# Performance work log

Measured on AMD Instinct MI355X. Metric: run time of the kernel, lower is better.

Reference implementation:

```python
import jax, jax.numpy as jnp
import numpy as np

B, T, D, H = 4, 1024, 1024, 16
NUM_BUCKETS = 320
MAX_DIST = 800
LN_EPS = 1e-5


def _rel_bucket(T):
    # bidirectional T5-style relative position buckets
    ctx = jnp.arange(T)[:, None]
    mem = jnp.arange(T)[None, :]
    rel = mem - ctx  # (T, T)
    half = NUM_BUCKETS // 2  # 160
    bucket = (rel > 0).astype(jnp.int32) * half
    n = jnp.abs(rel)
    max_exact = half // 2  # 80
    is_small = n < max_exact
    n_f = jnp.maximum(n, 1).astype(jnp.float32)
    large = max_exact + (
        jnp.log(n_f / max_exact) / np.log(MAX_DIST / max_exact) * (half - max_exact)
    ).astype(jnp.int32)
    large = jnp.minimum(large, half - 1)
    return bucket + jnp.where(is_small, n, large)


def setup_inputs() -> dict:
    key = jax.random.key(0)
    ks = jax.random.split(key, 12)
    s = 0.02
    return {
        "x": jax.random.normal(ks[0], (B, T, D), jnp.float32),
        "ln_w": jnp.ones((D,), jnp.float32),
        "ln_b": jnp.zeros((D,), jnp.float32),
        "wq": jax.random.normal(ks[1], (D, D), jnp.float32) * s,
        "bq": jnp.zeros((D,), jnp.float32),
        "wk": jax.random.normal(ks[2], (D, D), jnp.float32) * s,
        "bk": jnp.zeros((D,), jnp.float32),
        "wv": jax.random.normal(ks[3], (D, D), jnp.float32) * s,
        "bv": jnp.zeros((D,), jnp.float32),
        "wo": jax.random.normal(ks[4], (D, D), jnp.float32) * s,
        "bo": jnp.zeros((D,), jnp.float32),
        "rel_emb": jax.random.normal(ks[5], (NUM_BUCKETS, H), jnp.float32) * s,
        "grep_w": jax.random.normal(ks[6], (8, D // H), jnp.float32) * s,
        "grep_b": jnp.zeros((8,), jnp.float32),
        "grep_a": jnp.ones((1, H, 1, 1), jnp.float32),
    }


def reference(x, ln_w, ln_b, wq, bq, wk, bk, wv, bv, wo, bo, rel_emb, grep_w, grep_b, grep_a):
    Bb, Tt, Dd = x.shape
    hd = Dd // H
    scaling = hd ** -0.5
    # pre-norm LayerNorm
    mu = jnp.mean(x, -1, keepdims=True)
    var = jnp.mean((x - mu) ** 2, -1, keepdims=True)
    h = (x - mu) / jnp.sqrt(var + LN_EPS) * ln_w + ln_b
    # projections (q pre-scaled as in fairseq/WavLM)
    q = (h @ wq.T + bq) * scaling
    k = h @ wk.T + bk
    v = h @ wv.T + bv
    q = q.reshape(Bb, Tt, H, hd).transpose(0, 2, 1, 3)  # (B,H,T,hd)
    k = k.reshape(Bb, Tt, H, hd).transpose(0, 2, 1, 3)
    v = v.reshape(Bb, Tt, H, hd).transpose(0, 2, 1, 3)
    # bucketed relative position bias: (H, T, T)
    buckets = _rel_bucket(Tt)
    pos_bias = rel_emb[buckets].transpose(2, 0, 1)
    # gru_rel_pos gating (per batch, head, query position)
    alpha = 32.0
    ql = q * (alpha / scaling)  # undo scaling, multiply by alpha
    g = jax.nn.sigmoid((ql @ grep_w.T + grep_b).reshape(Bb, H, Tt, 2, 4).sum(-1))
    gate_a, gate_b = g[..., 0:1], g[..., 1:2]  # (B,H,T,1)
    gate = gate_a * (gate_b * grep_a - 1.0) + 2.0
    # attention
    scores = jnp.einsum('bhtd,bhsd->bhts', q, k) + gate * pos_bias[None]
    attn = jax.nn.softmax(scores, axis=-1)
    out = jnp.einsum('bhts,bhsd->bhtd', attn, v).transpose(0, 2, 1, 3).reshape(Bb, Tt, Dd)
    # output projection, dropout (identity in eval), residual
    out = out @ wo.T + bo + x
    pos_bias_out = jnp.broadcast_to(pos_bias[None], (Bb, H, Tt, Tt)).reshape(Bb * H, Tt, Tt)
    return out, pos_bias_out
```

## Files before the change

### kernel.cpp

```cpp
#include <hip/hip_runtime.h>

typedef unsigned short u16;
typedef __attribute__((ext_vector_type(8))) short short8;
typedef __attribute__((ext_vector_type(4))) float floatx4;

#define MFMA16(a, b, c) __builtin_amdgcn_mfma_f32_16x16x32_bf16(a, b, c, 0, 0, 0)

#define GLL16(gp, lp)                                                              \
  __builtin_amdgcn_global_load_lds(                                                \
      (const __attribute__((address_space(1))) void*)(gp),                         \
      (__attribute__((address_space(3))) void*)(lp), 16, 0, 0)

__device__ __forceinline__ float bf2f(u16 u) {
  return __uint_as_float(((unsigned int)u) << 16);
}
__device__ __forceinline__ u16 f2bf(float f) {
  unsigned int u = __float_as_uint(f);
  unsigned int r = (u + 0x7fffu + ((u >> 16) & 1u)) >> 16;
  return (u16)r;
}

__global__ __launch_bounds__(256) void ln_kernel(
    const float* __restrict__ x, const float* __restrict__ w, const float* __restrict__ bb,
    u16* __restrict__ hb)
{
  int wid = threadIdx.x >> 6, lane = threadIdx.x & 63;
  int row = blockIdx.x * 4 + wid;
  const float* xr = x + row * 1024 + lane * 16;
  float xs[16];
#pragma unroll
  for (int i = 0; i < 4; i++) {
    float4 v = *(const float4*)(xr + i * 4);
    xs[i * 4 + 0] = v.x; xs[i * 4 + 1] = v.y; xs[i * 4 + 2] = v.z; xs[i * 4 + 3] = v.w;
  }
  float s = 0.f, ss = 0.f;
#pragma unroll
  for (int i = 0; i < 16; i++) { s += xs[i]; ss += xs[i] * xs[i]; }
#pragma unroll
  for (int m = 1; m < 64; m <<= 1) { s += __shfl_xor(s, m, 64); ss += __shfl_xor(ss, m, 64); }
  float mu = s * (1.0f / 1024.0f);
  float var = ss * (1.0f / 1024.0f) - mu * mu;
  float rstd = rsqrtf(var + 1e-5f);
  const float* wr = w + lane * 16;
  const float* br = bb + lane * 16;
  short8 o0, o1;
#pragma unroll
  for (int i = 0; i < 8; i++) {
    o0[i] = (short)f2bf((xs[i] - mu) * rstd * wr[i] + br[i]);
    o1[i] = (short)f2bf((xs[8 + i] - mu) * rstd * wr[8 + i] + br[8 + i]);
  }
  u16* hr = hb + row * 1024 + lane * 16;
  *(short8*)hr = o0;
  *(short8*)(hr + 8) = o1;
}

__device__ __forceinline__ int rel_bucket(int t, int s) {
  int rel = s - t;
  int bucket = (rel > 0) ? 160 : 0;
  int n = (rel < 0) ? -rel : rel;
  if (n < 80) return bucket + n;
  float a = logf((float)n / 80.0f);
  float c = a / (float)2.302585092994046;
  float v = c * 80.0f;
  int large = 80 + (int)v;
  if (large > 159) large = 159;
  return bucket + large;
}

__global__ __launch_bounds__(256) void convw_kernel(
    const float* __restrict__ wq, const float* __restrict__ wk,
    const float* __restrict__ wv, const float* __restrict__ wo,
    u16* __restrict__ wb, const float* __restrict__ rel_emb, float* __restrict__ tbl)
{
  int bid = blockIdx.x;
  if (bid >= 2048) {
    int idx = (bid - 2048) * 256 + threadIdx.x;
    int h = idx & 15, ri = idx >> 4;
    float v = 0.f;
    if (ri < 2047) {
      int rel = ri - 1023;
      v = rel_emb[rel_bucket(0, rel) * 16 + h];
    }
    tbl[h * 2048 + ri] = v;
    return;
  }
  int idx = (bid * 256 + threadIdx.x) * 8;
  int seg = idx >> 20, off = idx & 1048575;
  const float* s = (seg == 0) ? wq : (seg == 1) ? wk : (seg == 2) ? wv : wo;
  float4 f0 = *(const float4*)(s + off);
  float4 f1 = *(const float4*)(s + off + 4);
  short8 o;
  o[0] = (short)f2bf(f0.x); o[1] = (short)f2bf(f0.y);
  o[2] = (short)f2bf(f0.z); o[3] = (short)f2bf(f0.w);
  o[4] = (short)f2bf(f1.x); o[5] = (short)f2bf(f1.y);
  o[6] = (short)f2bf(f1.z); o[7] = (short)f2bf(f1.w);
  *(short8*)&wb[idx] = o;
}

__global__ __launch_bounds__(256) void qkv_kernel(
    const u16* __restrict__ hb, const u16* __restrict__ wb,
    const float* __restrict__ bq, const float* __restrict__ bk, const float* __restrict__ bv,
    u16* __restrict__ qs, u16* __restrict__ kko, u16* __restrict__ vn)
{
  __shared__ __align__(16) u16 As[128 * 32];
  __shared__ __align__(16) u16 Bs[128 * 32];
  int tid = threadIdx.x;
  int wid = tid >> 6, lane = tid & 63;
  int wm = wid >> 1, wn = wid & 1;
  int l15 = lane & 15, quad = lane >> 4;
  int m0 = blockIdx.y * 128;
  int n0g = blockIdx.x * 128;
  int sec = n0g >> 10;
  int n0 = n0g & 1023;
  const u16* W = wb + sec * 1048576;
  const float* bias = (sec == 0) ? bq : ((sec == 1) ? bk : bv);

  floatx4 zero4 = {0.f, 0.f, 0.f, 0.f};
  floatx4 acc[4][4];
#pragma unroll
  for (int i = 0; i < 4; i++)
#pragma unroll
    for (int j = 0; j < 4; j++) acc[i][j] = zero4;

  int lr = tid >> 2;
  int lc = (tid & 3) * 8;
  const u16* ga0 = &hb[(m0 + lr) * 1024 + lc];
  const u16* ga1 = &hb[(m0 + lr + 64) * 1024 + lc];
  const u16* gb0 = &W[(n0 + lr) * 1024 + lc];
  const u16* gb1 = &W[(n0 + lr + 64) * 1024 + lc];
  u16* la0 = &As[lr * 32 + lc];
  u16* la1 = &As[(lr + 64) * 32 + lc];
  u16* lb0 = &Bs[lr * 32 + lc];
  u16* lb1 = &Bs[(lr + 64) * 32 + lc];

  for (int kt = 0; kt < 1024; kt += 32) {
    GLL16(ga0 + kt, la0);
    GLL16(ga1 + kt, la1);
    GLL16(gb0 + kt, lb0);
    GLL16(gb1 + kt, lb1);
    __syncthreads();
    short8 af[4], bf[4];
#pragma unroll
    for (int mi = 0; mi < 4; mi++)
      af[mi] = *(const short8*)&As[(wm * 64 + mi * 16 + l15) * 32 + quad * 8];
#pragma unroll
    for (int ni = 0; ni < 4; ni++)
      bf[ni] = *(const short8*)&Bs[(wn * 64 + ni * 16 + l15) * 32 + quad * 8];
#pragma unroll
    for (int mi = 0; mi < 4; mi++)
#pragma unroll
      for (int ni = 0; ni < 4; ni++)
        acc[mi][ni] = MFMA16(af[mi], bf[ni], acc[mi][ni]);
    __syncthreads();
  }

  int bidx = m0 >> 10;
#pragma unroll
  for (int mi = 0; mi < 4; mi++) {
#pragma unroll
    for (int ni = 0; ni < 4; ni++) {
#pragma unroll
      for (int r = 0; r < 4; r++) {
        int row = m0 + wm * 64 + mi * 16 + quad * 4 + r;
        int t = row & 1023;
        int c = n0 + wn * 64 + ni * 16 + l15;
        float val = acc[mi][ni][r] + bias[c];
        int hh = c >> 6, hp = c & 63;
        if (sec == 0) {
          val *= 0.125f;
          qs[((bidx * 16 + hh) * 1024 + t) * 64 + hp] = f2bf(val);
        } else if (sec == 1) {
          kko[((bidx * 16 + hh) * 1024 + t) * 64 + hp] = f2bf(val);
        } else {
          vn[((bidx * 16 + hh) * 1024 + t) * 64 + hp] = f2bf(val);
        }
      }
    }
  }
}

__global__ __launch_bounds__(256) void vtrans_kernel(
    const u16* __restrict__ vn, u16* __restrict__ vt)
{
  __shared__ u16 Ts[64 * 72];
  int bh = blockIdx.x >> 4;
  int t0 = (blockIdx.x & 15) * 64;
  int tid = threadIdx.x;
  int row = tid >> 2;
  int c16 = (tid & 3) * 16;
  const u16* src = vn + bh * 65536 + (t0 + row) * 64 + c16;
  *(short8*)&Ts[row * 72 + c16]     = *(const short8*)&src[0];
  *(short8*)&Ts[row * 72 + c16 + 8] = *(const short8*)&src[8];
  __syncthreads();
  short8 o0, o1;
#pragma unroll
  for (int j = 0; j < 8; j++) {
    o0[j] = (short)Ts[(c16 + j) * 72 + row];
    o1[j] = (short)Ts[(c16 + 8 + j) * 72 + row];
  }
  u16* dst = vt + bh * 65536 + row * 1024 + t0 + c16;
  *(short8*)&dst[0] = o0;
  *(short8*)&dst[8] = o1;
}

__global__ __launch_bounds__(256) void attn_kernel(
    const u16* __restrict__ qs, const u16* __restrict__ kko, const u16* __restrict__ vt,
    const float* __restrict__ gw, const float* __restrict__ gb, const float* __restrict__ ga,
    const float* __restrict__ tbl, u16* __restrict__ ao)
{
  __shared__ __align__(16) u16 Pb[4][2 * 768];
  int wid = threadIdx.x >> 6, lane = threadIdx.x & 63;
  int l15 = lane & 15, quad = lane >> 4;
  int bh = blockIdx.x;
  int b = bh >> 4, h = bh & 15;
  int q0 = blockIdx.y * 64 + wid * 16;
  const u16* Q = qs + bh * 65536;
  const u16* K = kko + bh * 65536;
  const u16* V = vt + bh * 65536;
  u16* pbase = &Pb[wid][0];

  const u16* qrow = Q + (q0 + l15) * 64;
  float e[8];
#pragma unroll
  for (int i = 0; i < 8; i++) e[i] = 0.f;
  {
    short8 qa = *(const short8*)&qrow[quad * 16];
    short8 qc = *(const short8*)&qrow[quad * 16 + 8];
#pragma unroll
    for (int jj = 0; jj < 8; jj++) {
      float qla = bf2f((u16)qa[jj]) * 256.0f;
      float qlb = bf2f((u16)qc[jj]) * 256.0f;
      int j = quad * 16 + jj;
#pragma unroll
      for (int i = 0; i < 8; i++) {
        e[i] += qla * gw[i * 64 + j];
        e[i] += qlb * gw[i * 64 + j + 8];
      }
    }
  }
#pragma unroll
  for (int i = 0; i < 8; i++) {
    e[i] += __shfl_xor(e[i], 16, 64);
    e[i] += __shfl_xor(e[i], 32, 64);
  }
  float u0 = e[0] + e[1] + e[2] + e[3] + gb[0] + gb[1] + gb[2] + gb[3];
  float u1 = e[4] + e[5] + e[6] + e[7] + gb[4] + gb[5] + gb[6] + gb[7];
  float sa = 1.0f / (1.0f + __expf(-u0));
  float sc_ = 1.0f / (1.0f + __expf(-u1));
  float gv = sa * (sc_ * ga[h] - 1.0f) + 2.0f;

  short8 qf0 = *(const short8*)&Q[(q0 + l15) * 64 + quad * 8];
  short8 qf1 = *(const short8*)&Q[(q0 + l15) * 64 + quad * 8 + 32];

  const float* tb = tbl + h * 2048 + 1023 + quad * 4 - (q0 + l15);

  float mrun = -1e30f, lrun = 0.f;
  floatx4 zero4 = {0.f, 0.f, 0.f, 0.f};
  floatx4 accO[4];
#pragma unroll
  for (int ni = 0; ni < 4; ni++) accO[ni] = zero4;

  const u16* Kr = K + l15 * 64 + quad * 8;
  short8 ka0 = *(const short8*)&Kr[0];
  short8 ka1 = *(const short8*)&Kr[32];
  short8 kb0 = *(const short8*)&Kr[16 * 64];
  short8 kb1 = *(const short8*)&Kr[16 * 64 + 32];
  float bt[8];
#pragma unroll
  for (int r = 0; r < 4; r++) { bt[r] = tb[r]; bt[4 + r] = tb[16 + r]; }

  for (int it = 0; it < 32; it++) {
    int s0 = it * 32;
    floatx4 sc0 = zero4, sc1 = zero4;
    sc0 = MFMA16(ka0, qf0, sc0);
    sc0 = MFMA16(ka1, qf1, sc0);
    sc1 = MFMA16(kb0, qf0, sc1);
    sc1 = MFMA16(kb1, qf1, sc1);

    int sn = (s0 + 32) & 1023;
    const u16* Kn = K + (sn + l15) * 64 + quad * 8;
    short8 na0 = *(const short8*)&Kn[0];
    short8 na1 = *(const short8*)&Kn[32];
    short8 nb0 = *(const short8*)&Kn[16 * 64];
    short8 nb1 = *(const short8*)&Kn[16 * 64 + 32];
    float btn[8];
#pragma unroll
    for (int r = 0; r < 4; r++) { btn[r] = tb[sn + r]; btn[4 + r] = tb[sn + 16 + r]; }
    short8 vf0 = *(const short8*)&V[(0 * 16 + l15) * 1024 + s0 + quad * 8];
    short8 vf1 = *(const short8*)&V[(1 * 16 + l15) * 1024 + s0 + quad * 8];
    short8 vf2 = *(const short8*)&V[(2 * 16 + l15) * 1024 + s0 + quad * 8];
    short8 vf3 = *(const short8*)&V[(3 * 16 + l15) * 1024 + s0 + quad * 8];

    float vv[8];
#pragma unroll
    for (int r = 0; r < 4; r++) {
      vv[r]     = sc0[r] + gv * bt[r];
      vv[4 + r] = sc1[r] + gv * bt[4 + r];
    }
    float mt = fmaxf(fmaxf(fmaxf(vv[0], vv[1]), fmaxf(vv[2], vv[3])),
                     fmaxf(fmaxf(vv[4], vv[5]), fmaxf(vv[6], vv[7])));
    mt = fmaxf(mt, __shfl_xor(mt, 16, 64));
    mt = fmaxf(mt, __shfl_xor(mt, 32, 64));
    float mnew = fmaxf(mrun, mt);
    float al = __expf(fmaxf(mrun - mnew, -80.0f));
    float p[8], ps = 0.f;
#pragma unroll
    for (int j = 0; j < 8; j++) { p[j] = __expf(vv[j] - mnew); ps += p[j]; }
    ps += __shfl_xor(ps, 16, 64);
    ps += __shfl_xor(ps, 32, 64);
    lrun = lrun * al + ps;
    mrun = mnew;

    float ar[4];
#pragma unroll
    for (int r = 0; r < 4; r++) ar[r] = __shfl(al, quad * 4 + r, 64);
#pragma unroll
    for (int ni = 0; ni < 4; ni++) {
      floatx4 t = accO[ni];
      t[0] *= ar[0]; t[1] *= ar[1]; t[2] *= ar[2]; t[3] *= ar[3];
      accO[ni] = t;
    }

    unsigned w0, w1, w2, w3;
    asm("v_cvt_pk_bf16_f32 %0, %1, %2" : "=v"(w0) : "v"(p[0]), "v"(p[1]));
    asm("v_cvt_pk_bf16_f32 %0, %1, %2" : "=v"(w1) : "v"(p[2]), "v"(p[3]));
    asm("v_cvt_pk_bf16_f32 %0, %1, %2" : "=v"(w2) : "v"(p[4]), "v"(p[5]));
    asm("v_cvt_pk_bf16_f32 %0, %1, %2" : "=v"(w3) : "v"(p[6]), "v"(p[7]));
    u16* pw = pbase + (it & 1) * 768;
    uint2 wa; wa.x = w0; wa.y = w1;
    uint2 wbv; wbv.x = w2; wbv.y = w3;
    *(uint2*)&pw[l15 * 48 + quad * 4] = wa;
    *(uint2*)&pw[l15 * 48 + 16 + quad * 4] = wbv;
    asm volatile("s_waitcnt lgkmcnt(0)" ::: "memory");
    __builtin_amdgcn_sched_barrier(0);
    short8 pf = *(const short8*)&pw[l15 * 48 + quad * 8];

    accO[0] = MFMA16(pf, vf0, accO[0]);
    accO[1] = MFMA16(pf, vf1, accO[1]);
    accO[2] = MFMA16(pf, vf2, accO[2]);
    accO[3] = MFMA16(pf, vf3, accO[3]);

    ka0 = na0; ka1 = na1; kb0 = nb0; kb1 = nb1;
#pragma unroll
    for (int j = 0; j < 8; j++) bt[j] = btn[j];
  }

#pragma unroll
  for (int r = 0; r < 4; r++) {
    float lr = __shfl(lrun, quad * 4 + r, 64);
    float rl = 1.0f / lr;
    int t = q0 + quad * 4 + r;
#pragma unroll
    for (int ni = 0; ni < 4; ni++) {
      ao[(b * 1024 + t) * 1024 + h * 64 + ni * 16 + l15] = f2bf(accO[ni][r] * rl);
    }
  }
}

__global__ __launch_bounds__(256) void oproj_kernel(
    const u16* __restrict__ ao, const u16* __restrict__ wob, const float* __restrict__ bo,
    const float* __restrict__ x, float* __restrict__ out)
{
  __shared__ __align__(16) u16 As[128 * 32];
  __shared__ __align__(16) u16 Bs[128 * 32];
  int tid = threadIdx.x;
  int wid = tid >> 6, lane = tid & 63;
  int wm = wid >> 1, wn = wid & 1;
  int l15 = lane & 15, quad = lane >> 4;
  int m0 = blockIdx.y * 128;
  int n0 = blockIdx.x * 128;

  floatx4 zero4 = {0.f, 0.f, 0.f, 0.f};
  floatx4 acc[4][4];
#pragma unroll
  for (int i = 0; i < 4; i++)
#pragma unroll
    for (int j = 0; j < 4; j++) acc[i][j] = zero4;

  int lr = tid >> 2;
  int lc = (tid & 3) * 8;
  const u16* ga0 = &ao[(m0 + lr) * 1024 + lc];
  const u16* ga1 = &ao[(m0 + lr + 64) * 1024 + lc];
  const u16* gb0 = &wob[(n0 + lr) * 1024 + lc];
  const u16* gb1 = &wob[(n0 + lr + 64) * 1024 + lc];
  u16* la0 = &As[lr * 32 + lc];
  u16* la1 = &As[(lr + 64) * 32 + lc];
  u16* lb0 = &Bs[lr * 32 + lc];
  u16* lb1 = &Bs[(lr + 64) * 32 + lc];

  for (int kt = 0; kt < 1024; kt += 32) {
    GLL16(ga0 + kt, la0);
    GLL16(ga1 + kt, la1);
    GLL16(gb0 + kt, lb0);
    GLL16(gb1 + kt, lb1);
    __syncthreads();
    short8 af[4], bf[4];
#pragma unroll
    for (int mi = 0; mi < 4; mi++)
      af[mi] = *(const short8*)&As[(wm * 64 + mi * 16 + l15) * 32 + quad * 8];
#pragma unroll
    for (int ni = 0; ni < 4; ni++)
      bf[ni] = *(const short8*)&Bs[(wn * 64 + ni * 16 + l15) * 32 + quad * 8];
#pragma unroll
    for (int mi = 0; mi < 4; mi++)
#pragma unroll
      for (int ni = 0; ni < 4; ni++)
        acc[mi][ni] = MFMA16(af[mi], bf[ni], acc[mi][ni]);
    __syncthreads();
  }

#pragma unroll
  for (int mi = 0; mi < 4; mi++) {
#pragma unroll
    for (int ni = 0; ni < 4; ni++) {
#pragma unroll
      for (int r = 0; r < 4; r++) {
        int row = m0 + wm * 64 + mi * 16 + quad * 4 + r;
        int c = n0 + wn * 64 + ni * 16 + l15;
        out[row * 1024 + c] = acc[mi][ni][r] + bo[c] + x[row * 1024 + c];
      }
    }
  }
}

__global__ __launch_bounds__(256) void bias_all_kernel(
    const float* __restrict__ rel_emb, float* __restrict__ out1)
{
  int tid = blockIdx.x * 256 + threadIdx.x;
  int t = tid >> 7;
  int s0 = (tid & 127) * 8;
  int bkt[8];
#pragma unroll
  for (int j = 0; j < 8; j++) bkt[j] = rel_bucket(t, s0 + j) * 16;
  int base_ts = t * 1024 + s0;
#pragma unroll
  for (int hh = 0; hh < 16; hh++) {
    float4 v0, v1;
    v0.x = rel_emb[bkt[0] + hh]; v0.y = rel_emb[bkt[1] + hh];
    v0.z = rel_emb[bkt[2] + hh]; v0.w = rel_emb[bkt[3] + hh];
    v1.x = rel_emb[bkt[4] + hh]; v1.y = rel_emb[bkt[5] + hh];
    v1.z = rel_emb[bkt[6] + hh]; v1.w = rel_emb[bkt[7] + hh];
    float* p = out1 + hh * 1048576 + base_ts;
    *(float4*)p = v0;              *(float4*)(p + 4) = v1;
    *(float4*)(p + 16777216) = v0; *(float4*)(p + 16777216 + 4) = v1;
    *(float4*)(p + 33554432) = v0; *(float4*)(p + 33554432 + 4) = v1;
    *(float4*)(p + 50331648) = v0; *(float4*)(p + 50331648 + 4) = v1;
  }
}

extern "C" void kernel_launch(void* const* d_in, const int* in_sizes, int n_in,
                              void* d_out, int out_size, void* d_ws, size_t ws_size,
                              hipStream_t stream) {
  const float* x    = (const float*)d_in[0];
  const float* ln_w = (const float*)d_in[1];
  const float* ln_b = (const float*)d_in[2];
  const float* wq   = (const float*)d_in[3];
  const float* bq   = (const float*)d_in[4];
  const float* wk   = (const float*)d_in[5];
  const float* bk   = (const float*)d_in[6];
  const float* wv   = (const float*)d_in[7];
  const float* bv   = (const float*)d_in[8];
  const float* wo   = (const float*)d_in[9];
  const float* bo   = (const float*)d_in[10];
  const float* rel  = (const float*)d_in[11];
  const float* gw   = (const float*)d_in[12];
  const float* gb   = (const float*)d_in[13];
  const float* ga   = (const float*)d_in[14];

  float* out0  = (float*)d_out;
  float* out1f = out0 + 4194304;

  u16* hbb  = (u16*)(out1f + 16777216);
  u16* wbb  = (u16*)(out1f + 18874368);
  u16* qsb  = (u16*)(out1f + 20971520);
  u16* kkb  = (u16*)(out1f + 23068672);
  u16* vnb  = (u16*)(out1f + 25165824);
  u16* vtb  = (u16*)(out1f + 27262976);
  u16* aob  = (u16*)(out1f + 29360128);
  float* tbl =        out1f + 31457280;

  ln_kernel<<<1024, 256, 0, stream>>>(x, ln_w, ln_b, hbb);
  convw_kernel<<<2176, 256, 0, stream>>>(wq, wk, wv, wo, wbb, rel, tbl);
  qkv_kernel<<<dim3(24, 32), 256, 0, stream>>>(hbb, wbb, bq, bk, bv, qsb, kkb, vnb);
  vtrans_kernel<<<1024, 256, 0, stream>>>(vnb, vtb);
  attn_kernel<<<dim3(64, 16), 256, 0, stream>>>(qsb, kkb, vtb, gw, gb, ga, tbl, aob);
  oproj_kernel<<<dim3(8, 32), 256, 0, stream>>>(aob, wbb + 3145728, bo, x, out0);
  bias_all_kernel<<<512, 256, 0, stream>>>(rel, out1f);
}
```

Baseline: 524.6 us.

## Fold positional-bias output writes into QKV and attention kernels as extra blocks

When the workspace is large enough, intermediates move from the tail of the output buffer into the workspace. The standalone bias broadcast kernel, which writes 256 MB, is then split across extra blocks appended to the QKV GEMM grid (256 blocks) and the attention grid (256 blocks). The aim is to overlap the bandwidth-bound bias stores with compute-bound GEMM and attention work and to remove one launch. The risk is that the store traffic competes with the compute blocks for memory bandwidth and cache. If the workspace is too small, the old path runs unchanged.

```diff
diff --git a/kernel.cpp b/kernel.cpp
--- a/kernel.cpp
+++ b/kernel.cpp
@@ -18,40 +18,6 @@
   unsigned int u = __float_as_uint(f);
   unsigned int r = (u + 0x7fffu + ((u >> 16) & 1u)) >> 16;
   return (u16)r;
-}
-
-__global__ __launch_bounds__(256) void ln_kernel(
-    const float* __restrict__ x, const float* __restrict__ w, const float* __restrict__ bb,
-    u16* __restrict__ hb)
-{
-  int wid = threadIdx.x >> 6, lane = threadIdx.x & 63;
-  int row = blockIdx.x * 4 + wid;
-  const float* xr = x + row * 1024 + lane * 16;
-  float xs[16];
-#pragma unroll
-  for (int i = 0; i < 4; i++) {
-    float4 v = *(const float4*)(xr + i * 4);
-    xs[i * 4 + 0] = v.x; xs[i * 4 + 1] = v.y; xs[i * 4 + 2] = v.z; xs[i * 4 + 3] = v.w;
-  }
-  float s = 0.f, ss = 0.f;
-#pragma unroll
-  for (int i = 0; i < 16; i++) { s += xs[i]; ss += xs[i] * xs[i]; }
-#pragma unroll
-  for (int m = 1; m < 64; m <<= 1) { s += __shfl_xor(s, m, 64); ss += __shfl_xor(ss, m, 64); }
-  float mu = s * (1.0f / 1024.0f);
-  float var = ss * (1.0f / 1024.0f) - mu * mu;
-  float rstd = rsqrtf(var + 1e-5f);
-  const float* wr = w + lane * 16;
-  const float* br = bb + lane * 16;
-  short8 o0, o1;
-#pragma unroll
-  for (int i = 0; i < 8; i++) {
-    o0[i] = (short)f2bf((xs[i] - mu) * rstd * wr[i] + br[i]);
-    o1[i] = (short)f2bf((xs[8 + i] - mu) * rstd * wr[8 + i] + br[8 + i]);
-  }
-  u16* hr = hb + row * 1024 + lane * 16;
-  *(short8*)hr = o0;
-  *(short8*)(hr + 8) = o1;
 }
 
 __device__ __forceinline__ int rel_bucket(int t, int s) {
@@ -67,6 +33,65 @@
   return bucket + large;
 }
 
+__device__ __forceinline__ void bias_slice(int bid, const float* __restrict__ rel_emb,
+                                           float* __restrict__ out1)
+{
+  int tid = bid * 256 + threadIdx.x;
+  int t = tid >> 7;
+  int s0 = (tid & 127) * 8;
+  int bkt[8];
+#pragma unroll
+  for (int j = 0; j < 8; j++) bkt[j] = rel_bucket(t, s0 + j) * 16;
+  int base_ts = t * 1024 + s0;
+#pragma unroll
+  for (int hh = 0; hh < 16; hh++) {
+    float4 v0, v1;
+    v0.x = rel_emb[bkt[0] + hh]; v0.y = rel_emb[bkt[1] + hh];
+    v0.z = rel_emb[bkt[2] + hh]; v0.w = rel_emb[bkt[3] + hh];
+    v1.x = rel_emb[bkt[4] + hh]; v1.y = rel_emb[bkt[5] + hh];
+    v1.z = rel_emb[bkt[6] + hh]; v1.w = rel_emb[bkt[7] + hh];
+    float* p = out1 + hh * 1048576 + base_ts;
+    *(float4*)p = v0;              *(float4*)(p + 4) = v1;
+    *(float4*)(p + 16777216) = v0; *(float4*)(p + 16777216 + 4) = v1;
+    *(float4*)(p + 33554432) = v0; *(float4*)(p + 33554432 + 4) = v1;
+    *(float4*)(p + 50331648) = v0; *(float4*)(p + 50331648 + 4) = v1;
+  }
+}
+
+__global__ __launch_bounds__(256) void ln_kernel(
+    const float* __restrict__ x, const float* __restrict__ w, const float* __restrict__ bb,
+    u16* __restrict__ hb)
+{
+  int wid = threadIdx.x >> 6, lane = threadIdx.x & 63;
+  int row = blockIdx.x * 4 + wid;
+  const float* xr = x + row * 1024 + lane * 16;
+  float xs[16];
+#pragma unroll
+  for (int i = 0; i < 4; i++) {
+    float4 v = *(const float4*)(xr + i * 4);
+    xs[i * 4 + 0] = v.x; xs[i * 4 + 1] = v.y; xs[i * 4 + 2] = v.z; xs[i * 4 + 3] = v.w;
+  }
+  float s = 0.f, ss = 0.f;
+#pragma unroll
+  for (int i = 0; i < 16; i++) { s += xs[i]; ss += xs[i] * xs[i]; }
+#pragma unroll
+  for (int m = 1; m < 64; m <<= 1) { s += __shfl_xor(s, m, 64); ss += __shfl_xor(ss, m, 64); }
+  float mu = s * (1.0f / 1024.0f);
+  float var = ss * (1.0f / 1024.0f) - mu * mu;
+  float rstd = rsqrtf(var + 1e-5f);
+  const float* wr = w + lane * 16;
+  const float* br = bb + lane * 16;
+  short8 o0, o1;
+#pragma unroll
+  for (int i = 0; i < 8; i++) {
+    o0[i] = (short)f2bf((xs[i] - mu) * rstd * wr[i] + br[i]);
+    o1[i] = (short)f2bf((xs[8 + i] - mu) * rstd * wr[8 + i] + br[8 + i]);
+  }
+  u16* hr = hb + row * 1024 + lane * 16;
+  *(short8*)hr = o0;
+  *(short8*)(hr + 8) = o1;
+}
+
 __global__ __launch_bounds__(256) void convw_kernel(
     const float* __restrict__ wq, const float* __restrict__ wk,
     const float* __restrict__ wv, const float* __restrict__ wo,
@@ -100,10 +125,15 @@
 __global__ __launch_bounds__(256) void qkv_kernel(
     const u16* __restrict__ hb, const u16* __restrict__ wb,
     const float* __restrict__ bq, const float* __restrict__ bk, const float* __restrict__ bv,
-    u16* __restrict__ qs, u16* __restrict__ kko, u16* __restrict__ vn)
+    u16* __restrict__ qs, u16* __restrict__ kko, u16* __restrict__ vn,
+    const float* __restrict__ rel_emb, float* __restrict__ out1)
 {
   __shared__ __align__(16) u16 As[128 * 32];
   __shared__ __align__(16) u16 Bs[128 * 32];
+  if (blockIdx.x >= 24) {
+    bias_slice((blockIdx.x - 24) * gridDim.y + blockIdx.y, rel_emb, out1);
+    return;
+  }
   int tid = threadIdx.x;
   int wid = tid >> 6, lane = tid & 63;
   int wm = wid >> 1, wn = wid & 1;
@@ -206,9 +236,14 @@
 __global__ __launch_bounds__(256) void attn_kernel(
     const u16* __restrict__ qs, const u16* __restrict__ kko, const u16* __restrict__ vt,
     const float* __restrict__ gw, const float* __restrict__ gb, const float* __restrict__ ga,
-    const float* __restrict__ tbl, u16* __restrict__ ao)
+    const float* __restrict__ tbl, u16* __restrict__ ao,
+    const float* __restrict__ rel_emb, float* __restrict__ out1)
 {
   __shared__ __align__(16) u16 Pb[4][2 * 768];
+  if (blockIdx.x >= 64) {
+    bias_slice(256 + (blockIdx.x - 64) * gridDim.y + blockIdx.y, rel_emb, out1);
+    return;
+  }
   int wid = threadIdx.x >> 6, lane = threadIdx.x & 63;
   int l15 = lane & 15, quad = lane >> 4;
   int bh = blockIdx.x;
@@ -426,26 +461,7 @@
 __global__ __launch_bounds__(256) void bias_all_kernel(
     const float* __restrict__ rel_emb, float* __restrict__ out1)
 {
-  int tid = blockIdx.x * 256 + threadIdx.x;
-  int t = tid >> 7;
-  int s0 = (tid & 127) * 8;
-  int bkt[8];
-#pragma unroll
-  for (int j = 0; j < 8; j++) bkt[j] = rel_bucket(t, s0 + j) * 16;
-  int base_ts = t * 1024 + s0;
-#pragma unroll
-  for (int hh = 0; hh < 16; hh++) {
-    float4 v0, v1;
-    v0.x = rel_emb[bkt[0] + hh]; v0.y = rel_emb[bkt[1] + hh];
-    v0.z = rel_emb[bkt[2] + hh]; v0.w = rel_emb[bkt[3] + hh];
-    v1.x = rel_emb[bkt[4] + hh]; v1.y = rel_emb[bkt[5] + hh];
-    v1.z = rel_emb[bkt[6] + hh]; v1.w = rel_emb[bkt[7] + hh];
-    float* p = out1 + hh * 1048576 + base_ts;
-    *(float4*)p = v0;              *(float4*)(p + 4) = v1;
-    *(float4*)(p + 16777216) = v0; *(float4*)(p + 16777216 + 4) = v1;
-    *(float4*)(p + 33554432) = v0; *(float4*)(p + 33554432 + 4) = v1;
-    *(float4*)(p + 50331648) = v0; *(float4*)(p + 50331648 + 4) = v1;
-  }
+  bias_slice(blockIdx.x, rel_emb, out1);
 }
 
 extern "C" void kernel_launch(void* const* d_in, const int* in_sizes, int n_in,
@@ -470,20 +486,30 @@
   float* out0  = (float*)d_out;
   float* out1f = out0 + 4194304;
 
-  u16* hbb  = (u16*)(out1f + 16777216);
-  u16* wbb  = (u16*)(out1f + 18874368);
-  u16* qsb  = (u16*)(out1f + 20971520);
-  u16* kkb  = (u16*)(out1f + 23068672);
-  u16* vnb  = (u16*)(out1f + 25165824);
-  u16* vtb  = (u16*)(out1f + 27262976);
-  u16* aob  = (u16*)(out1f + 29360128);
-  float* tbl =        out1f + 31457280;
+  bool use_ws = (ws_size >= (size_t)(64u << 20));
+  float* scr = use_ws ? (float*)d_ws : (out1f + 16777216);
+
+  u16* hbb  = (u16*)(scr);
+  u16* wbb  = (u16*)(scr + 2097152);
+  u16* qsb  = (u16*)(scr + 4194304);
+  u16* kkb  = (u16*)(scr + 6291456);
+  u16* vnb  = (u16*)(scr + 8388608);
+  u16* vtb  = (u16*)(scr + 10485760);
+  u16* aob  = (u16*)(scr + 12582912);
+  float* tbl =        scr + 14680064;
 
   ln_kernel<<<1024, 256, 0, stream>>>(x, ln_w, ln_b, hbb);
   convw_kernel<<<2176, 256, 0, stream>>>(wq, wk, wv, wo, wbb, rel, tbl);
-  qkv_kernel<<<dim3(24, 32), 256, 0, stream>>>(hbb, wbb, bq, bk, bv, qsb, kkb, vnb);
-  vtrans_kernel<<<1024, 256, 0, stream>>>(vnb, vtb);
-  attn_kernel<<<dim3(64, 16), 256, 0, stream>>>(qsb, kkb, vtb, gw, gb, ga, tbl, aob);
-  oproj_kernel<<<dim3(8, 32), 256, 0, stream>>>(aob, wbb + 3145728, bo, x, out0);
-  bias_all_kernel<<<512, 256, 0, stream>>>(rel, out1f);
-}
+  if (use_ws) {
+    qkv_kernel<<<dim3(32, 32), 256, 0, stream>>>(hbb, wbb, bq, bk, bv, qsb, kkb, vnb, rel, out1f);
+    vtrans_kernel<<<1024, 256, 0, stream>>>(vnb, vtb);
+    attn_kernel<<<dim3(80, 16), 256, 0, stream>>>(qsb, kkb, vtb, gw, gb, ga, tbl, aob, rel, out1f);
+    oproj_kernel<<<dim3(8, 32), 256, 0, stream>>>(aob, wbb + 3145728, bo, x, out0);
+  } else {
+    qkv_kernel<<<dim3(24, 32), 256, 0, stream>>>(hbb, wbb, bq, bk, bv, qsb, kkb, vnb, rel, out1f);
+    vtrans_kernel<<<1024, 256, 0, stream>>>(vnb, vtb);
+    attn_kernel<<<dim3(64, 16), 256, 0, stream>>>(qsb, kkb, vtb, gw, gb, ga, tbl, aob, rel, out1f);
+    oproj_kernel<<<dim3(8, 32), 256, 0, stream>>>(aob, wbb + 3145728, bo, x, out0);
+    bias_all_kernel<<<512, 256, 0, stream>>>(rel, out1f);
+  }
+}
```

Result: slower. 560.3 us (+6.8%).

## Process 64 keys per attention iteration with lazy softmax rescaling

Applied to the files above, without the earlier changes.

The attention loop now handles 64 keys per iteration instead of 32, with two K fragment sets prefetched in a rotating fashion and twice as many V fragments loaded per step. The online softmax skips the max update and accumulator rescale when every lane's new tile max stays within 8 of the running max. The kernel gains a launch-bounds occupancy hint of 4, and scratch buffers move to the workspace when it is large enough. The intent is to cut per-key loop overhead, shuffles and rescale multiplies, at the cost of more registers and a larger LDS P buffer.

```diff
diff --git a/kernel.cpp b/kernel.cpp
--- a/kernel.cpp
+++ b/kernel.cpp
@@ -18,40 +18,6 @@
   unsigned int u = __float_as_uint(f);
   unsigned int r = (u + 0x7fffu + ((u >> 16) & 1u)) >> 16;
   return (u16)r;
-}
-
-__global__ __launch_bounds__(256) void ln_kernel(
-    const float* __restrict__ x, const float* __restrict__ w, const float* __restrict__ bb,
-    u16* __restrict__ hb)
-{
-  int wid = threadIdx.x >> 6, lane = threadIdx.x & 63;
-  int row = blockIdx.x * 4 + wid;
-  const float* xr = x + row * 1024 + lane * 16;
-  float xs[16];
-#pragma unroll
-  for (int i = 0; i < 4; i++) {
-    float4 v = *(const float4*)(xr + i * 4);
-    xs[i * 4 + 0] = v.x; xs[i * 4 + 1] = v.y; xs[i * 4 + 2] = v.z; xs[i * 4 + 3] = v.w;
-  }
-  float s = 0.f, ss = 0.f;
-#pragma unroll
-  for (int i = 0; i < 16; i++) { s += xs[i]; ss += xs[i] * xs[i]; }
-#pragma unroll
-  for (int m = 1; m < 64; m <<= 1) { s += __shfl_xor(s, m, 64); ss += __shfl_xor(ss, m, 64); }
-  float mu = s * (1.0f / 1024.0f);
-  float var = ss * (1.0f / 1024.0f) - mu * mu;
-  float rstd = rsqrtf(var + 1e-5f);
-  const float* wr = w + lane * 16;
-  const float* br = bb + lane * 16;
-  short8 o0, o1;
-#pragma unroll
-  for (int i = 0; i < 8; i++) {
-    o0[i] = (short)f2bf((xs[i] - mu) * rstd * wr[i] + br[i]);
-    o1[i] = (short)f2bf((xs[8 + i] - mu) * rstd * wr[8 + i] + br[8 + i]);
-  }
-  u16* hr = hb + row * 1024 + lane * 16;
-  *(short8*)hr = o0;
-  *(short8*)(hr + 8) = o1;
 }
 
 __device__ __forceinline__ int rel_bucket(int t, int s) {
@@ -65,6 +31,40 @@
   int large = 80 + (int)v;
   if (large > 159) large = 159;
   return bucket + large;
+}
+
+__global__ __launch_bounds__(256) void ln_kernel(
+    const float* __restrict__ x, const float* __restrict__ w, const float* __restrict__ bb,
+    u16* __restrict__ hb)
+{
+  int wid = threadIdx.x >> 6, lane = threadIdx.x & 63;
+  int row = blockIdx.x * 4 + wid;
+  const float* xr = x + row * 1024 + lane * 16;
+  float xs[16];
+#pragma unroll
+  for (int i = 0; i < 4; i++) {
+    float4 v = *(const float4*)(xr + i * 4);
+    xs[i * 4 + 0] = v.x; xs[i * 4 + 1] = v.y; xs[i * 4 + 2] = v.z; xs[i * 4 + 3] = v.w;
+  }
+  float s = 0.f, ss = 0.f;
+#pragma unroll
+  for (int i = 0; i < 16; i++) { s += xs[i]; ss += xs[i] * xs[i]; }
+#pragma unroll
+  for (int m = 1; m < 64; m <<= 1) { s += __shfl_xor(s, m, 64); ss += __shfl_xor(ss, m, 64); }
+  float mu = s * (1.0f / 1024.0f);
+  float var = ss * (1.0f / 1024.0f) - mu * mu;
+  float rstd = rsqrtf(var + 1e-5f);
+  const float* wr = w + lane * 16;
+  const float* br = bb + lane * 16;
+  short8 o0, o1;
+#pragma unroll
+  for (int i = 0; i < 8; i++) {
+    o0[i] = (short)f2bf((xs[i] - mu) * rstd * wr[i] + br[i]);
+    o1[i] = (short)f2bf((xs[8 + i] - mu) * rstd * wr[8 + i] + br[8 + i]);
+  }
+  u16* hr = hb + row * 1024 + lane * 16;
+  *(short8*)hr = o0;
+  *(short8*)(hr + 8) = o1;
 }
 
 __global__ __launch_bounds__(256) void convw_kernel(
@@ -203,12 +203,12 @@
   *(short8*)&dst[8] = o1;
 }
 
-__global__ __launch_bounds__(256) void attn_kernel(
+__global__ __launch_bounds__(256, 4) void attn_kernel(
     const u16* __restrict__ qs, const u16* __restrict__ kko, const u16* __restrict__ vt,
     const float* __restrict__ gw, const float* __restrict__ gb, const float* __restrict__ ga,
     const float* __restrict__ tbl, u16* __restrict__ ao)
 {
-  __shared__ __align__(16) u16 Pb[4][2 * 768];
+  __shared__ __align__(16) u16 Pb[4][2 * 1152];
   int wid = threadIdx.x >> 6, lane = threadIdx.x & 63;
   int l15 = lane & 15, quad = lane >> 4;
   int bh = blockIdx.x;
@@ -260,89 +260,108 @@
 #pragma unroll
   for (int ni = 0; ni < 4; ni++) accO[ni] = zero4;
 
-  const u16* Kr = K + l15 * 64 + quad * 8;
-  short8 ka0 = *(const short8*)&Kr[0];
-  short8 ka1 = *(const short8*)&Kr[32];
-  short8 kb0 = *(const short8*)&Kr[16 * 64];
-  short8 kb1 = *(const short8*)&Kr[16 * 64 + 32];
-  float bt[8];
-#pragma unroll
-  for (int r = 0; r < 4; r++) { bt[r] = tb[r]; bt[4 + r] = tb[16 + r]; }
-
-  for (int it = 0; it < 32; it++) {
-    int s0 = it * 32;
-    floatx4 sc0 = zero4, sc1 = zero4;
-    sc0 = MFMA16(ka0, qf0, sc0);
-    sc0 = MFMA16(ka1, qf1, sc0);
-    sc1 = MFMA16(kb0, qf0, sc1);
-    sc1 = MFMA16(kb1, qf1, sc1);
-
-    int sn = (s0 + 32) & 1023;
-    const u16* Kn = K + (sn + l15) * 64 + quad * 8;
-    short8 na0 = *(const short8*)&Kn[0];
-    short8 na1 = *(const short8*)&Kn[32];
-    short8 nb0 = *(const short8*)&Kn[16 * 64];
-    short8 nb1 = *(const short8*)&Kn[16 * 64 + 32];
-    float btn[8];
-#pragma unroll
-    for (int r = 0; r < 4; r++) { btn[r] = tb[sn + r]; btn[4 + r] = tb[sn + 16 + r]; }
-    short8 vf0 = *(const short8*)&V[(0 * 16 + l15) * 1024 + s0 + quad * 8];
-    short8 vf1 = *(const short8*)&V[(1 * 16 + l15) * 1024 + s0 + quad * 8];
-    short8 vf2 = *(const short8*)&V[(2 * 16 + l15) * 1024 + s0 + quad * 8];
-    short8 vf3 = *(const short8*)&V[(3 * 16 + l15) * 1024 + s0 + quad * 8];
-
-    float vv[8];
+  const u16* Kq8 = K + quad * 8;
+  short8 kc0 = *(const short8*)&Kq8[(0 + l15) * 64];
+  short8 kc1 = *(const short8*)&Kq8[(0 + l15) * 64 + 32];
+  short8 kc2 = *(const short8*)&Kq8[(16 + l15) * 64];
+  short8 kc3 = *(const short8*)&Kq8[(16 + l15) * 64 + 32];
+  short8 kn0 = *(const short8*)&Kq8[(32 + l15) * 64];
+  short8 kn1 = *(const short8*)&Kq8[(32 + l15) * 64 + 32];
+  short8 kn2 = *(const short8*)&Kq8[(48 + l15) * 64];
+  short8 kn3 = *(const short8*)&Kq8[(48 + l15) * 64 + 32];
+
+  for (int it = 0; it < 16; it++) {
+    int s0 = it * 64;
+    floatx4 sA0 = zero4, sA1 = zero4, sB0 = zero4, sB1 = zero4;
+    sA0 = MFMA16(kc0, qf0, sA0); sA0 = MFMA16(kc1, qf1, sA0);
+    sA1 = MFMA16(kc2, qf0, sA1); sA1 = MFMA16(kc3, qf1, sA1);
+    {
+      int sn = (s0 + 64) & 1023;
+      const u16* KA = K + (sn + l15) * 64 + quad * 8;
+      kc0 = *(const short8*)&KA[0];
+      kc1 = *(const short8*)&KA[32];
+      kc2 = *(const short8*)&KA[16 * 64];
+      kc3 = *(const short8*)&KA[16 * 64 + 32];
+    }
+    sB0 = MFMA16(kn0, qf0, sB0); sB0 = MFMA16(kn1, qf1, sB0);
+    sB1 = MFMA16(kn2, qf0, sB1); sB1 = MFMA16(kn3, qf1, sB1);
+    {
+      int sn = (s0 + 96) & 1023;
+      const u16* KB = K + (sn + l15) * 64 + quad * 8;
+      kn0 = *(const short8*)&KB[0];
+      kn1 = *(const short8*)&KB[32];
+      kn2 = *(const short8*)&KB[16 * 64];
+      kn3 = *(const short8*)&KB[16 * 64 + 32];
+    }
+    short8 vfA[4], vfB[4];
+#pragma unroll
+    for (int ni = 0; ni < 4; ni++) {
+      vfA[ni] = *(const short8*)&V[(ni * 16 + l15) * 1024 + s0 + quad * 8];
+      vfB[ni] = *(const short8*)&V[(ni * 16 + l15) * 1024 + s0 + 32 + quad * 8];
+    }
+
+    float vv[16];
 #pragma unroll
     for (int r = 0; r < 4; r++) {
-      vv[r]     = sc0[r] + gv * bt[r];
-      vv[4 + r] = sc1[r] + gv * bt[4 + r];
-    }
-    float mt = fmaxf(fmaxf(fmaxf(vv[0], vv[1]), fmaxf(vv[2], vv[3])),
-                     fmaxf(fmaxf(vv[4], vv[5]), fmaxf(vv[6], vv[7])));
+      vv[r]      = sA0[r] + gv * tb[s0 + r];
+      vv[4 + r]  = sA1[r] + gv * tb[s0 + 16 + r];
+      vv[8 + r]  = sB0[r] + gv * tb[s0 + 32 + r];
+      vv[12 + r] = sB1[r] + gv * tb[s0 + 48 + r];
+    }
+    float m0v = fmaxf(fmaxf(fmaxf(vv[0], vv[1]), fmaxf(vv[2], vv[3])),
+                      fmaxf(fmaxf(vv[4], vv[5]), fmaxf(vv[6], vv[7])));
+    float m1v = fmaxf(fmaxf(fmaxf(vv[8], vv[9]), fmaxf(vv[10], vv[11])),
+                      fmaxf(fmaxf(vv[12], vv[13]), fmaxf(vv[14], vv[15])));
+    float mt = fmaxf(m0v, m1v);
     mt = fmaxf(mt, __shfl_xor(mt, 16, 64));
     mt = fmaxf(mt, __shfl_xor(mt, 32, 64));
-    float mnew = fmaxf(mrun, mt);
-    float al = __expf(fmaxf(mrun - mnew, -80.0f));
-    float p[8], ps = 0.f;
-#pragma unroll
-    for (int j = 0; j < 8; j++) { p[j] = __expf(vv[j] - mnew); ps += p[j]; }
-    ps += __shfl_xor(ps, 16, 64);
-    ps += __shfl_xor(ps, 32, 64);
-    lrun = lrun * al + ps;
-    mrun = mnew;
-
-    float ar[4];
-#pragma unroll
-    for (int r = 0; r < 4; r++) ar[r] = __shfl(al, quad * 4 + r, 64);
-#pragma unroll
-    for (int ni = 0; ni < 4; ni++) {
-      floatx4 t = accO[ni];
-      t[0] *= ar[0]; t[1] *= ar[1]; t[2] *= ar[2]; t[3] *= ar[3];
-      accO[ni] = t;
-    }
-
-    unsigned w0, w1, w2, w3;
-    asm("v_cvt_pk_bf16_f32 %0, %1, %2" : "=v"(w0) : "v"(p[0]), "v"(p[1]));
-    asm("v_cvt_pk_bf16_f32 %0, %1, %2" : "=v"(w1) : "v"(p[2]), "v"(p[3]));
-    asm("v_cvt_pk_bf16_f32 %0, %1, %2" : "=v"(w2) : "v"(p[4]), "v"(p[5]));
-    asm("v_cvt_pk_bf16_f32 %0, %1, %2" : "=v"(w3) : "v"(p[6]), "v"(p[7]));
-    u16* pw = pbase + (it & 1) * 768;
-    uint2 wa; wa.x = w0; wa.y = w1;
-    uint2 wbv; wbv.x = w2; wbv.y = w3;
-    *(uint2*)&pw[l15 * 48 + quad * 4] = wa;
-    *(uint2*)&pw[l15 * 48 + 16 + quad * 4] = wbv;
+
+    float p[16], ps = 0.f;
+    if (__all(mt - mrun <= 8.0f)) {
+#pragma unroll
+      for (int j = 0; j < 16; j++) { p[j] = __expf(vv[j] - mrun); ps += p[j]; }
+      ps += __shfl_xor(ps, 16, 64);
+      ps += __shfl_xor(ps, 32, 64);
+      lrun += ps;
+    } else {
+      float mnew = fmaxf(mrun, mt);
+      float al = __expf(fmaxf(mrun - mnew, -80.0f));
+#pragma unroll
+      for (int j = 0; j < 16; j++) { p[j] = __expf(vv[j] - mnew); ps += p[j]; }
+      ps += __shfl_xor(ps, 16, 64);
+      ps += __shfl_xor(ps, 32, 64);
+      lrun = lrun * al + ps;
+      mrun = mnew;
+      float ar[4];
+#pragma unroll
+      for (int r = 0; r < 4; r++) ar[r] = __shfl(al, quad * 4 + r, 64);
+#pragma unroll
+      for (int ni = 0; ni < 4; ni++) {
+        floatx4 t = accO[ni];
+        t[0] *= ar[0]; t[1] *= ar[1]; t[2] *= ar[2]; t[3] *= ar[3];
+        accO[ni] = t;
+      }
+    }
+
+    u16* pw = pbase + (it & 1) * 1152;
+#pragma unroll
+    for (int g = 0; g < 4; g++) {
+      unsigned w0, w1;
+      asm("v_cvt_pk_bf16_f32 %0, %1, %2" : "=v"(w0) : "v"(p[4 * g + 0]), "v"(p[4 * g + 1]));
+      asm("v_cvt_pk_bf16_f32 %0, %1, %2" : "=v"(w1) : "v"(p[4 * g + 2]), "v"(p[4 * g + 3]));
+      uint2 wv_; wv_.x = w0; wv_.y = w1;
+      *(uint2*)&pw[l15 * 72 + g * 16 + quad * 4] = wv_;
+    }
     asm volatile("s_waitcnt lgkmcnt(0)" ::: "memory");
     __builtin_amdgcn_sched_barrier(0);
-    short8 pf = *(const short8*)&pw[l15 * 48 + quad * 8];
-
-    accO[0] = MFMA16(pf, vf0, accO[0]);
-    accO[1] = MFMA16(pf, vf1, accO[1]);
-    accO[2] = MFMA16(pf, vf2, accO[2]);
-    accO[3] = MFMA16(pf, vf3, accO[3]);
-
-    ka0 = na0; ka1 = na1; kb0 = nb0; kb1 = nb1;
-#pragma unroll
-    for (int j = 0; j < 8; j++) bt[j] = btn[j];
+    short8 pf0 = *(const short8*)&pw[l15 * 72 + quad * 8];
+    short8 pf1 = *(const short8*)&pw[l15 * 72 + 32 + quad * 8];
+
+#pragma unroll
+    for (int ni = 0; ni < 4; ni++) {
+      accO[ni] = MFMA16(pf0, vfA[ni], accO[ni]);
+      accO[ni] = MFMA16(pf1, vfB[ni], accO[ni]);
+    }
   }
 
 #pragma unroll
@@ -470,14 +489,17 @@
   float* out0  = (float*)d_out;
   float* out1f = out0 + 4194304;
 
-  u16* hbb  = (u16*)(out1f + 16777216);
-  u16* wbb  = (u16*)(out1f + 18874368);
-  u16* qsb  = (u16*)(out1f + 20971520);
-  u16* kkb  = (u16*)(out1f + 23068672);
-  u16* vnb  = (u16*)(out1f + 25165824);
-  u16* vtb  = (u16*)(out1f + 27262976);
-  u16* aob  = (u16*)(out1f + 29360128);
-  float* tbl =        out1f + 31457280;
+  bool use_ws = (ws_size >= (size_t)(64u << 20));
+  float* scr = use_ws ? (float*)d_ws : (out1f + 16777216);
+
+  u16* hbb  = (u16*)(scr);
+  u16* wbb  = (u16*)(scr + 2097152);
+  u16* qsb  = (u16*)(scr + 4194304);
+  u16* kkb  = (u16*)(scr + 6291456);
+  u16* vnb  = (u16*)(scr + 8388608);
+  u16* vtb  = (u16*)(scr + 10485760);
+  u16* aob  = (u16*)(scr + 12582912);
+  float* tbl =        scr + 14680064;
 
   ln_kernel<<<1024, 256, 0, stream>>>(x, ln_w, ln_b, hbb);
   convw_kernel<<<2176, 256, 0, stream>>>(wq, wk, wv, wo, wbb, rel, tbl);
```

New measurement: 535.9 us. 2.2% more time.

## Split attention over two key halves and merge partial softmax results

Applied to the files above, without the earlier changes.

The attention kernel now splits the key/value range into two halves, so the grid doubles and each block runs half as many iterations. Each half writes unnormalised fp32 output plus its running max and sum, and a new merge kernel rescales and combines them into the bf16 attention output. The aim is more independent waves in flight to hide latency in the serial key loop. In exchange it adds a launch and extra fp32 global traffic for the partial results. Intermediate buffers also move to the workspace when it is large enough.

```diff
diff --git a/kernel.cpp b/kernel.cpp
--- a/kernel.cpp
+++ b/kernel.cpp
@@ -18,40 +18,6 @@
   unsigned int u = __float_as_uint(f);
   unsigned int r = (u + 0x7fffu + ((u >> 16) & 1u)) >> 16;
   return (u16)r;
-}
-
-__global__ __launch_bounds__(256) void ln_kernel(
-    const float* __restrict__ x, const float* __restrict__ w, const float* __restrict__ bb,
-    u16* __restrict__ hb)
-{
-  int wid = threadIdx.x >> 6, lane = threadIdx.x & 63;
-  int row = blockIdx.x * 4 + wid;
-  const float* xr = x + row * 1024 + lane * 16;
-  float xs[16];
-#pragma unroll
-  for (int i = 0; i < 4; i++) {
-    float4 v = *(const float4*)(xr + i * 4);
-    xs[i * 4 + 0] = v.x; xs[i * 4 + 1] = v.y; xs[i * 4 + 2] = v.z; xs[i * 4 + 3] = v.w;
-  }
-  float s = 0.f, ss = 0.f;
-#pragma unroll
-  for (int i = 0; i < 16; i++) { s += xs[i]; ss += xs[i] * xs[i]; }
-#pragma unroll
-  for (int m = 1; m < 64; m <<= 1) { s += __shfl_xor(s, m, 64); ss += __shfl_xor(ss, m, 64); }
-  float mu = s * (1.0f / 1024.0f);
-  float var = ss * (1.0f / 1024.0f) - mu * mu;
-  float rstd = rsqrtf(var + 1e-5f);
-  const float* wr = w + lane * 16;
-  const float* br = bb + lane * 16;
-  short8 o0, o1;
-#pragma unroll
-  for (int i = 0; i < 8; i++) {
-    o0[i] = (short)f2bf((xs[i] - mu) * rstd * wr[i] + br[i]);
-    o1[i] = (short)f2bf((xs[8 + i] - mu) * rstd * wr[8 + i] + br[8 + i]);
-  }
-  u16* hr = hb + row * 1024 + lane * 16;
-  *(short8*)hr = o0;
-  *(short8*)(hr + 8) = o1;
 }
 
 __device__ __forceinline__ int rel_bucket(int t, int s) {
@@ -65,6 +31,40 @@
   int large = 80 + (int)v;
   if (large > 159) large = 159;
   return bucket + large;
+}
+
+__global__ __launch_bounds__(256) void ln_kernel(
+    const float* __restrict__ x, const float* __restrict__ w, const float* __restrict__ bb,
+    u16* __restrict__ hb)
+{
+  int wid = threadIdx.x >> 6, lane = threadIdx.x & 63;
+  int row = blockIdx.x * 4 + wid;
+  const float* xr = x + row * 1024 + lane * 16;
+  float xs[16];
+#pragma unroll
+  for (int i = 0; i < 4; i++) {
+    float4 v = *(const float4*)(xr + i * 4);
+    xs[i * 4 + 0] = v.x; xs[i * 4 + 1] = v.y; xs[i * 4 + 2] = v.z; xs[i * 4 + 3] = v.w;
+  }
+  float s = 0.f, ss = 0.f;
+#pragma unroll
+  for (int i = 0; i < 16; i++) { s += xs[i]; ss += xs[i] * xs[i]; }
+#pragma unroll
+  for (int m = 1; m < 64; m <<= 1) { s += __shfl_xor(s, m, 64); ss += __shfl_xor(ss, m, 64); }
+  float mu = s * (1.0f / 1024.0f);
+  float var = ss * (1.0f / 1024.0f) - mu * mu;
+  float rstd = rsqrtf(var + 1e-5f);
+  const float* wr = w + lane * 16;
+  const float* br = bb + lane * 16;
+  short8 o0, o1;
+#pragma unroll
+  for (int i = 0; i < 8; i++) {
+    o0[i] = (short)f2bf((xs[i] - mu) * rstd * wr[i] + br[i]);
+    o1[i] = (short)f2bf((xs[8 + i] - mu) * rstd * wr[8 + i] + br[8 + i]);
+  }
+  u16* hr = hb + row * 1024 + lane * 16;
+  *(short8*)hr = o0;
+  *(short8*)(hr + 8) = o1;
 }
 
 __global__ __launch_bounds__(256) void convw_kernel(
@@ -206,14 +206,16 @@
 __global__ __launch_bounds__(256) void attn_kernel(
     const u16* __restrict__ qs, const u16* __restrict__ kko, const u16* __restrict__ vt,
     const float* __restrict__ gw, const float* __restrict__ gb, const float* __restrict__ ga,
-    const float* __restrict__ tbl, u16* __restrict__ ao)
+    const float* __restrict__ tbl, float* __restrict__ Op, float* __restrict__ ml)
 {
   __shared__ __align__(16) u16 Pb[4][2 * 768];
   int wid = threadIdx.x >> 6, lane = threadIdx.x & 63;
   int l15 = lane & 15, quad = lane >> 4;
   int bh = blockIdx.x;
-  int b = bh >> 4, h = bh & 15;
-  int q0 = blockIdx.y * 64 + wid * 16;
+  int h = bh & 15;
+  int qt = blockIdx.y >> 1, half = blockIdx.y & 1;
+  int q0 = qt * 64 + wid * 16;
+  int sbase = half * 512;
   const u16* Q = qs + bh * 65536;
   const u16* K = kko + bh * 65536;
   const u16* V = vt + bh * 65536;
@@ -260,24 +262,24 @@
 #pragma unroll
   for (int ni = 0; ni < 4; ni++) accO[ni] = zero4;
 
-  const u16* Kr = K + l15 * 64 + quad * 8;
+  const u16* Kr = K + (sbase + l15) * 64 + quad * 8;
   short8 ka0 = *(const short8*)&Kr[0];
   short8 ka1 = *(const short8*)&Kr[32];
   short8 kb0 = *(const short8*)&Kr[16 * 64];
   short8 kb1 = *(const short8*)&Kr[16 * 64 + 32];
   float bt[8];
 #pragma unroll
-  for (int r = 0; r < 4; r++) { bt[r] = tb[r]; bt[4 + r] = tb[16 + r]; }
-
-  for (int it = 0; it < 32; it++) {
-    int s0 = it * 32;
+  for (int r = 0; r < 4; r++) { bt[r] = tb[sbase + r]; bt[4 + r] = tb[sbase + 16 + r]; }
+
+  for (int it = 0; it < 16; it++) {
+    int s0 = sbase + it * 32;
     floatx4 sc0 = zero4, sc1 = zero4;
     sc0 = MFMA16(ka0, qf0, sc0);
     sc0 = MFMA16(ka1, qf1, sc0);
     sc1 = MFMA16(kb0, qf0, sc1);
     sc1 = MFMA16(kb1, qf1, sc1);
 
-    int sn = (s0 + 32) & 1023;
+    int sn = sbase + ((it * 32 + 32) & 511);
     const u16* Kn = K + (sn + l15) * 64 + quad * 8;
     short8 na0 = *(const short8*)&Kn[0];
     short8 na1 = *(const short8*)&Kn[32];
@@ -345,16 +347,52 @@
     for (int j = 0; j < 8; j++) bt[j] = btn[j];
   }
 
+  int rowb = (half * 64 + bh) * 1024;
 #pragma unroll
   for (int r = 0; r < 4; r++) {
-    float lr = __shfl(lrun, quad * 4 + r, 64);
-    float rl = 1.0f / lr;
     int t = q0 + quad * 4 + r;
 #pragma unroll
     for (int ni = 0; ni < 4; ni++) {
-      ao[(b * 1024 + t) * 1024 + h * 64 + ni * 16 + l15] = f2bf(accO[ni][r] * rl);
-    }
-  }
+      Op[(rowb + t) * 64 + ni * 16 + l15] = accO[ni][r];
+    }
+  }
+  if (quad == 0) {
+    int t = q0 + l15;
+    ml[(rowb + t) * 2]     = mrun;
+    ml[(rowb + t) * 2 + 1] = lrun;
+  }
+}
+
+__global__ __launch_bounds__(256) void merge_kernel(
+    const float* __restrict__ Op, const float* __restrict__ ml, u16* __restrict__ ao)
+{
+  int idx = blockIdx.x * 256 + threadIdx.x;
+  int row = idx >> 3;
+  int hd0 = (idx & 7) * 8;
+  float2 v0 = *(const float2*)&ml[row * 2];
+  float2 v1 = *(const float2*)&ml[131072 + row * 2];
+  float m = fmaxf(v0.x, v1.x);
+  float e0 = __expf(v0.x - m), e1 = __expf(v1.x - m);
+  float rl = 1.0f / (v0.y * e0 + v1.y * e1);
+  float s0 = e0 * rl, s1 = e1 * rl;
+  const float* p0 = Op + row * 64 + hd0;
+  const float* p1 = p0 + 4194304;
+  float4 a0 = *(const float4*)p0;
+  float4 a1 = *(const float4*)(p0 + 4);
+  float4 b0 = *(const float4*)p1;
+  float4 b1 = *(const float4*)(p1 + 4);
+  int bh = row >> 10, t = row & 1023;
+  u16* d = ao + ((bh >> 4) * 1024 + t) * 1024 + (bh & 15) * 64 + hd0;
+  short8 o;
+  o[0] = (short)f2bf(a0.x * s0 + b0.x * s1);
+  o[1] = (short)f2bf(a0.y * s0 + b0.y * s1);
+  o[2] = (short)f2bf(a0.z * s0 + b0.z * s1);
+  o[3] = (short)f2bf(a0.w * s0 + b0.w * s1);
+  o[4] = (short)f2bf(a1.x * s0 + b1.x * s1);
+  o[5] = (short)f2bf(a1.y * s0 + b1.y * s1);
+  o[6] = (short)f2bf(a1.z * s0 + b1.z * s1);
+  o[7] = (short)f2bf(a1.w * s0 + b1.w * s1);
+  *(short8*)d = o;
 }
 
 __global__ __launch_bounds__(256) void oproj_kernel(
@@ -470,20 +508,26 @@
   float* out0  = (float*)d_out;
   float* out1f = out0 + 4194304;
 
-  u16* hbb  = (u16*)(out1f + 16777216);
-  u16* wbb  = (u16*)(out1f + 18874368);
-  u16* qsb  = (u16*)(out1f + 20971520);
-  u16* kkb  = (u16*)(out1f + 23068672);
-  u16* vnb  = (u16*)(out1f + 25165824);
-  u16* vtb  = (u16*)(out1f + 27262976);
-  u16* aob  = (u16*)(out1f + 29360128);
-  float* tbl =        out1f + 31457280;
+  bool use_ws = (ws_size >= (size_t)(128u << 20));
+  float* scr = use_ws ? (float*)d_ws : (out1f + 16777216);
+
+  u16* hbb  = (u16*)(scr);
+  u16* wbb  = (u16*)(scr + 2097152);
+  u16* qsb  = (u16*)(scr + 4194304);
+  u16* kkb  = (u16*)(scr + 6291456);
+  u16* vnb  = (u16*)(scr + 8388608);
+  u16* vtb  = (u16*)(scr + 10485760);
+  u16* aob  = (u16*)(scr + 12582912);
+  float* tbl =        scr + 14680064;
+  float* Opb =        scr + 16777216;
+  float* mlb =        scr + 25165824;
 
   ln_kernel<<<1024, 256, 0, stream>>>(x, ln_w, ln_b, hbb);
   convw_kernel<<<2176, 256, 0, stream>>>(wq, wk, wv, wo, wbb, rel, tbl);
   qkv_kernel<<<dim3(24, 32), 256, 0, stream>>>(hbb, wbb, bq, bk, bv, qsb, kkb, vnb);
   vtrans_kernel<<<1024, 256, 0, stream>>>(vnb, vtb);
-  attn_kernel<<<dim3(64, 16), 256, 0, stream>>>(qsb, kkb, vtb, gw, gb, ga, tbl, aob);
+  attn_kernel<<<dim3(64, 32), 256, 0, stream>>>(qsb, kkb, vtb, gw, gb, ga, tbl, Opb, mlb);
+  merge_kernel<<<2048, 256, 0, stream>>>(Opb, mlb, aob);
   oproj_kernel<<<dim3(8, 32), 256, 0, stream>>>(aob, wbb + 3145728, bo, x, out0);
   bias_all_kernel<<<512, 256, 0, stream>>>(rel, out1f);
 }
```

Result: slower. 543.8 us (+3.7%).
